# Optimization experiments

Measured on AMD Instinct MI355X. Metric: run time of the kernel, lower is better.

The kernel has to match this reference:

```python
import jax, jax.numpy as jnp
import numpy as np

B, T, V, H, C = 128, 4096, 128, 256, 10
EPS = 0.1  # args._epsilon (training mode)

def setup_inputs() -> dict:
    key = jax.random.key(0)
    ks = jax.random.split(key, 8)
    rn = lambda k, shape, sc: (jax.random.normal(k, shape, jnp.float32) * sc)
    return {
        "X": rn(ks[0], (B, T, V), 1.0),
        "u": jax.random.uniform(ks[1], (B, T, 1), jnp.float32),
        "Wk": rn(ks[2], (V, 4 * H), 0.05),
        "Wr": rn(ks[3], (H, 4 * H), 0.05),
        "b_lstm": jnp.zeros((4 * H,), jnp.float32),
        "Wo": rn(ks[4], (H, C), 0.05),
        "bo": jnp.zeros((C,), jnp.float32),
        "Wc": rn(ks[5], (H + 1, 1), 0.05),
        "bc": jnp.zeros((1,), jnp.float32),
        "Wb": rn(ks[6], (H + 1, 1), 0.05),
        "bb": jnp.zeros((1,), jnp.float32),
    }

def reference(X, u, Wk, Wr, b_lstm, Wo, bo, Wc, bc, Wb, bb):
    Bn = X.shape[0]
    xT = jnp.swapaxes(X, 0, 1)  # [T,B,V]
    uT = jnp.swapaxes(u, 0, 1)  # [T,B,1]
    ts = jnp.arange(T, dtype=jnp.float32)

    def step(carry, inp):
        h, c, preds, halt = carry
        x_t, u_t, t = inp
        # Keras LSTMCell: gates order i, f, g(c), o
        z = x_t @ Wk + h @ Wr + b_lstm  # [B,4H]
        i, f, g, o = jnp.split(z, 4, axis=1)
        i = jax.nn.sigmoid(i); f = jax.nn.sigmoid(f)
        g = jnp.tanh(g); o = jax.nn.sigmoid(o)
        c = f * c + i * g
        h = o * jnp.tanh(c)
        logits = jax.nn.softmax(h @ Wo + bo, axis=-1)  # softmax Dense
        time = jnp.ones((Bn, 1), jnp.float32) * t
        c_in = jax.lax.stop_gradient(jnp.concatenate([h, time], axis=1))
        p = jax.nn.sigmoid(c_in @ Wc + bc)
        probs = (1.0 - EPS) * p + EPS * 0.05
        a = (u_t < probs).astype(jnp.float32)  # Bernoulli sample via uniform noise
        _b = c_in @ Wb + bb  # baseline (does not affect returned logits)
        preds = jnp.where((a == 1.0) & (preds == 0.0), logits, preds)
        halt = jnp.where((halt == -1.0) & (a == 1.0), time, halt)
        return (h, c, preds, halt), logits

    init = (jnp.zeros((Bn, H), jnp.float32),
            jnp.zeros((Bn, H), jnp.float32),
            jnp.zeros((Bn, C), jnp.float32),
            -jnp.ones((Bn, 1), jnp.float32))
    (h, c, preds, halt), all_logits = jax.lax.scan(step, init, (xT, uT, ts))
    logits_last = all_logits[-1]
    # samples that never halted get the final-step logits
    return jnp.where(preds == 0.0, logits_last, preds)
```

## Files before the change

### kernel.cpp

```cpp
#include <hip/hip_runtime.h>
#include <cstddef>
#include <cstdint>

#define NT_ 4096
#define NV_ 128
#define NH_ 256
#define NC_ 10
#define KT_ 384
#define NGRP 16
#define SB   8
#define GWG  16
#define TPW  256
#define VST  12
#define Z9   9
#define FULLMASK 255

#define SM_W    0
#define SM_V    24576
#define SM_ZP   (SM_V + KT_*VST)
#define SM_C    (SM_ZP + 2304)
#define SM_BL   (SM_C + 144)
#define SM_WC   (SM_BL + 64)
#define SM_WO   (SM_WC + 260)
#define SM_HD   (SM_WO + 2560)
#define SM_RED  (SM_HD + 12)
#define SM_TOT  (SM_RED + 32)
#define SMEM_BYTES (SM_TOT * 4)

#define WS_HBUF  4096
#define WS_DIAG  (1u << 20)

#define ALD(p)    __hip_atomic_load((p), __ATOMIC_RELAXED, __HIP_MEMORY_SCOPE_AGENT)
#define AST(p,v)  __hip_atomic_store((p), (v), __ATOMIC_RELAXED, __HIP_MEMORY_SCOPE_AGENT)

#define FMA8(S) \
  acc[S].x = fmaf(w4.x, vs, acc[S].x); \
  acc[S].y = fmaf(w4.y, vs, acc[S].y); \
  acc[S].z = fmaf(w4.z, vs, acc[S].z); \
  acc[S].w = fmaf(w4.w, vs, acc[S].w);

#define ZSTEP(i)                                            \
  {                                                         \
    float4 w4 = wl4[(i) * 256 + wbase];                     \
    const float* vk = v_lds + ((i) * 16 + ks) * VST;        \
    float4 va = *(const float4*)(vk);                       \
    float4 vb = *(const float4*)(vk + 4);                   \
    { float vs = va.x; FMA8(0) } { float vs = va.y; FMA8(1) } \
    { float vs = va.z; FMA8(2) } { float vs = va.w; FMA8(3) } \
    { float vs = vb.x; FMA8(4) } { float vs = vb.y; FMA8(5) } \
    { float vs = vb.z; FMA8(6) } { float vs = vb.w; FMA8(7) } \
  }

extern "C" __global__ __launch_bounds__(TPW, 1)
void earliest_coop(const float* __restrict__ X, const float* __restrict__ U,
                   const float* __restrict__ Wk, const float* __restrict__ Wr,
                   const float* __restrict__ bl, const float* __restrict__ Wo,
                   const float* __restrict__ bo, const float* __restrict__ Wc,
                   const float* __restrict__ bc, float* __restrict__ out,
                   int* __restrict__ cnt, float* __restrict__ hbuf,
                   char* __restrict__ diag)
{
  extern __shared__ float smem[];
  float* w_lds = smem + SM_W;
  float* v_lds = smem + SM_V;
  float* zp    = smem + SM_ZP;
  float* c_lds = smem + SM_C;
  float* bl_s  = smem + SM_BL;
  float* wc_s  = smem + SM_WC;
  float* wo_s  = smem + SM_WO;
  float* hd_s  = smem + SM_HD;
  float* red   = smem + SM_RED;
  __shared__ int halted_lds;
  __shared__ int wflags;

  const int tid  = threadIdx.x;
  const int w    = blockIdx.x & 15;
  const int g    = blockIdx.x >> 4;
  const int colq = tid & 15;
  const int ks   = tid >> 4;
  const bool leader = (w == 0);

  for (int m = 0; m < 24; ++m) {
    int idx4 = m * 256 + tid;
    int k = idx4 >> 4, cq = idx4 & 15;
    int rr = cq >> 2, qq = cq & 3;
    int col4 = rr * 64 + w * 4 + qq;
    float4 wv;
    if (k < NV_) wv = ((const float4*)Wk)[(size_t)k * 256 + col4];
    else         wv = ((const float4*)Wr)[(size_t)(k - NV_) * 256 + col4];
    ((float4*)w_lds)[k * 16 + (cq ^ (k & 7))] = wv;
  }
  if (tid < 64) {
    int rr = tid >> 4, e = tid & 15;
    bl_s[tid] = bl[rr * 256 + w * 16 + e];
  }
  wc_s[tid] = Wc[tid];
  if (tid == 0) wc_s[256] = Wc[256];
  if (tid < 128) c_lds[(tid >> 3) * Z9 + (tid & 7)] = 0.f;
  if (leader) {
    for (int m = tid; m < NH_ * NC_; m += TPW) wo_s[m] = Wo[m];
  }
  if (tid < 10)  hd_s[tid] = bo[tid];
  if (tid == 10) hd_s[10] = bc[0];
  if (tid == 0)  { halted_lds = 0; wflags = 0; }

  int* cntg = cnt + (g << 6);
  const int cswz  = colq ^ (ks & 7);
  const int wbase = ks * 16 + cswz;
  const float4* wl4 = (const float4*)w_lds;

  const int xk4 = tid >> 3;
  const int xs  = tid & 7;
  const float4* X4 = (const float4*)X;
  float4 xr = X4[((size_t)(g * SB + xs) * NT_ + 0) * 32 + xk4];

  __syncthreads();
  {
    #pragma unroll
    for (int j = 0; j < 4; ++j)
      v_lds[(4 * xk4 + j) * VST + xs] = ((const float*)&xr)[j];
  }
  __syncthreads();

  float4 acc[8];
  #pragma unroll
  for (int s = 0; s < 8; ++s) acc[s] = make_float4(0.f, 0.f, 0.f, 0.f);
  #pragma unroll
  for (int i = 0; i < 8; ++i) ZSTEP(i)

  float uv_pf = 0.f;

  for (int it = 0;; ++it) {
    if (tid == 0) wflags = 0;
    if (it == 0) {
      #pragma unroll
      for (int i2 = 0; i2 < 8; ++i2) {
        int flat = i2 * 256 + tid;
        v_lds[(NV_ + (flat >> 3)) * VST + (flat & 7)] = 0.f;
      }
    } else {
      const float* hsrc = hbuf + ((size_t)(it & 1) * NGRP + g) * NH_ * SB;
      #pragma unroll
      for (int i2 = 0; i2 < 8; ++i2) {
        int flat = i2 * 256 + tid;
        v_lds[(NV_ + (flat >> 3)) * VST + (flat & 7)] = ALD(hsrc + flat);
      }
    }
    __syncthreads();

    if (it < NT_) {
      if (it + 1 < NT_)
        xr = X4[((size_t)(g * SB + xs) * NT_ + (it + 1)) * 32 + xk4];
      #pragma unroll
      for (int i = 8; i < 24; ++i) ZSTEP(i)
      #pragma unroll
      for (int off = 16; off <= 32; off <<= 1) {
        #pragma unroll
        for (int s = 0; s < 8; ++s) {
          acc[s].x += __shfl_xor(acc[s].x, off, 64);
          acc[s].y += __shfl_xor(acc[s].y, off, 64);
          acc[s].z += __shfl_xor(acc[s].z, off, 64);
          acc[s].w += __shfl_xor(acc[s].w, off, 64);
        }
      }
      if ((tid & 48) == 0) {
        int w4 = tid >> 6;
        float4* zp4 = (float4*)zp;
        #pragma unroll
        for (int s = 0; s < 8; ++s) zp4[(w4 * 16 + colq) * Z9 + s] = acc[s];
      }
    }
    if (it >= 1) {
      const float* hv = v_lds + (NV_ + tid) * VST;
      const float wcv = wc_s[tid];
      float part[SB];
      #pragma unroll
      for (int s = 0; s < SB; ++s) part[s] = hv[s] * wcv;
      #pragma unroll
      for (int off = 1; off <= 32; off <<= 1) {
        #pragma unroll
        for (int s = 0; s < SB; ++s) part[s] += __shfl_xor(part[s], off, 64);
      }
      if ((tid & 63) == 0) {
        int w4 = tid >> 6;
        #pragma unroll
        for (int s = 0; s < SB; ++s) red[w4 * 8 + s] = part[s];
      }
      if (tid >= 128 && tid < 128 + SB)
        uv_pf = U[(size_t)(g * SB + (tid - 128)) * NT_ + (it - 1)];
    }
    __syncthreads();

    if (it < NT_ && tid < 128) {
      int e = tid >> 3, s = tid & 7;
      float zg4[4];
      #pragma unroll
      for (int r = 0; r < 4; ++r) {
        int cq = r * 4 + (e >> 2);
        int j  = e & 3;
        float sum = 0.f;
        #pragma unroll
        for (int w4 = 0; w4 < 4; ++w4)
          sum += zp[((w4 * 16 + cq) * Z9 + s) * 4 + j];
        zg4[r] = sum + bl_s[r * 16 + e];
      }
      float gi = 1.f / (1.f + expf(-zg4[0]));
      float gf = 1.f / (1.f + expf(-zg4[1]));
      float gg = tanhf(zg4[2]);
      float go = 1.f / (1.f + expf(-zg4[3]));
      float c = gf * c_lds[e * Z9 + s] + gi * gg;
      c_lds[e * Z9 + s] = c;
      float h = go * tanhf(c);
      size_t hidx = (((size_t)((it + 1) & 1) * NGRP + g) * NH_ + (w * 16 + e)) * SB + s;
      AST(hbuf + hidx, h);
    }
    if (it >= 1 && tid >= 128 && tid < 128 + SB) {
      const int s_ = tid - 128;
      if (!((halted_lds >> s_) & 1)) {
        const int tau = it - 1;
        const float psum = red[0 * 8 + s_] + red[1 * 8 + s_] + red[2 * 8 + s_] + red[3 * 8 + s_];
        const float pre   = psum + (float)tau * wc_s[256] + hd_s[10];
        const float p     = 1.f / (1.f + expf(-pre));
        const float probs = 0.9f * p + 0.005f;
        const bool  a     = (uv_pf < probs);
        if (a || tau == NT_ - 1) atomicOr(&wflags, 1 << s_);
        if (a) atomicOr(&halted_lds, 1 << s_);
      }
    }
    __syncthreads();

    if (tid == 0) {
      __hip_atomic_fetch_add(cntg, 1, __ATOMIC_RELAXED, __HIP_MEMORY_SCOPE_AGENT);
      if (diag)
        __builtin_nontemporal_store(1u,
            (uint32_t*)(diag + (((size_t)blockIdx.x << 8) + (it & 255)) * 64));
    }

    if (it + 1 < NT_) {
      #pragma unroll
      for (int j = 0; j < 4; ++j)
        v_lds[(4 * xk4 + j) * VST + xs] = ((const float*)&xr)[j];
    }

    if (it >= 1 && leader && wflags) {
      const int e5 = tid >> 3, s = tid & 7;
      float accv[NC_];
      #pragma unroll
      for (int cc = 0; cc < NC_; ++cc) accv[cc] = 0.f;
      #pragma unroll
      for (int i2 = 0; i2 < 8; ++i2) {
        const int e = i2 * 32 + e5;
        const float hvv = v_lds[(NV_ + e) * VST + s];
        #pragma unroll
        for (int cc = 0; cc < NC_; ++cc) accv[cc] += hvv * wo_s[e * NC_ + cc];
      }
      #pragma unroll
      for (int off = 8; off <= 32; off <<= 1) {
        #pragma unroll
        for (int cc = 0; cc < NC_; ++cc) accv[cc] += __shfl_xor(accv[cc], off, 64);
      }
      if ((tid & 56) == 0) {
        const int w4 = tid >> 6;
        #pragma unroll
        for (int cc = 0; cc < NC_; ++cc) zp[(w4 * 8 + s) * NC_ + cc] = accv[cc];
      }
      __syncthreads();
      if (tid < SB && ((wflags >> tid) & 1)) {
        const int s_ = tid;
        float l[NC_];
        float mx = -1e30f;
        #pragma unroll
        for (int cc = 0; cc < NC_; ++cc) {
          l[cc] = zp[(0 * 8 + s_) * NC_ + cc] + zp[(1 * 8 + s_) * NC_ + cc]
                + zp[(2 * 8 + s_) * NC_ + cc] + zp[(3 * 8 + s_) * NC_ + cc] + hd_s[cc];
          mx = fmaxf(mx, l[cc]);
        }
        float ssum = 0.f;
        #pragma unroll
        for (int cc = 0; cc < NC_; ++cc) { l[cc] = expf(l[cc] - mx); ssum += l[cc]; }
        const float inv = 1.f / ssum;
        float* op = out + (g * SB + s_) * NC_;
        #pragma unroll
        for (int cc = 0; cc < NC_; ++cc) op[cc] = l[cc] * inv;
      }
      __syncthreads();
    }

    if (halted_lds == FULLMASK || it == NT_) break;

    __syncthreads();

    #pragma unroll
    for (int s = 0; s < 8; ++s) acc[s] = make_float4(0.f, 0.f, 0.f, 0.f);
    if (it + 1 < NT_) {
      #pragma unroll
      for (int i = 0; i < 8; ++i) ZSTEP(i)
    }

    if (tid == 0) {
      const int target = GWG * (it + 1);
      while (ALD(cntg) < target) __builtin_amdgcn_s_sleep(1);
    }
    __syncthreads();
  }
}

extern "C" void kernel_launch(void* const* d_in, const int* in_sizes, int n_in,
                              void* d_out, int out_size, void* d_ws, size_t ws_size,
                              hipStream_t stream)
{
  const float* X  = (const float*)d_in[0];
  const float* U  = (const float*)d_in[1];
  const float* Wk = (const float*)d_in[2];
  const float* Wr = (const float*)d_in[3];
  const float* bL = (const float*)d_in[4];
  const float* Wo = (const float*)d_in[5];
  const float* bo = (const float*)d_in[6];
  const float* Wc = (const float*)d_in[7];
  const float* bc = (const float*)d_in[8];
  float* out = (float*)d_out;

  int*   cnt  = (int*)d_ws;
  float* hbuf = (float*)((char*)d_ws + WS_HBUF);
  char*  diag = (ws_size >= (6u << 20)) ? ((char*)d_ws + WS_DIAG) : nullptr;

  hipMemsetAsync(d_ws, 0, WS_HBUF, stream);

  hipFuncSetAttribute((const void*)earliest_coop,
                      hipFuncAttributeMaxDynamicSharedMemorySize, SMEM_BYTES);

  void* args[] = { (void*)&X, (void*)&U, (void*)&Wk, (void*)&Wr, (void*)&bL,
                   (void*)&Wo, (void*)&bo, (void*)&Wc, (void*)&bc, (void*)&out,
                   (void*)&cnt, (void*)&hbuf, (void*)&diag };
  hipError_t lerr = hipLaunchCooperativeKernel((const void*)earliest_coop,
                                               dim3(NGRP * GWG), dim3(TPW),
                                               args, SMEM_BYTES, stream);
  if (lerr != hipSuccess) {
    hipLaunchKernelGGL(earliest_coop, dim3(NGRP * GWG), dim3(TPW), SMEM_BYTES, stream,
                       X, U, Wk, Wr, bL, Wo, bo, Wc, bc, out, cnt, hbuf, diag);
  }
}
```

Baseline: 181.4 us.

## Replace group counter barrier with step-tagged hidden-state flags

The per-group atomic counter and spin barrier are replaced by 64-bit slots that pack each hidden value with its step index. Each thread polls only the eight values it needs until their tags match the current step, then writes them straight into LDS. This fuses data exchange and synchronisation into one round trip and removes the separate counter increment, its polling, and the reload pass at the top of each step. In exchange it moves twice the bytes per hidden value, every thread now spins on global memory instead of one, and correctness depends on the tag and data being written atomically in a single 64-bit store.

```diff
diff --git a/kernel.cpp b/kernel.cpp
--- a/kernel.cpp
+++ b/kernel.cpp
@@ -27,11 +27,11 @@
 #define SM_TOT  (SM_RED + 32)
 #define SMEM_BYTES (SM_TOT * 4)
 
-#define WS_HBUF  4096
-#define WS_DIAG  (1u << 20)
-
-#define ALD(p)    __hip_atomic_load((p), __ATOMIC_RELAXED, __HIP_MEMORY_SCOPE_AGENT)
-#define AST(p,v)  __hip_atomic_store((p), (v), __ATOMIC_RELAXED, __HIP_MEMORY_SCOPE_AGENT)
+#define WS_HQ_BYTES (512u * 1024u)
+#define WS_DIAG     (1u << 20)
+
+#define AQLD(p)   __hip_atomic_load((p),  __ATOMIC_RELAXED, __HIP_MEMORY_SCOPE_AGENT)
+#define AQST(p,v) __hip_atomic_store((p), (v), __ATOMIC_RELAXED, __HIP_MEMORY_SCOPE_AGENT)
 
 #define FMA8(S) \
   acc[S].x = fmaf(w4.x, vs, acc[S].x); \
@@ -57,8 +57,7 @@
                    const float* __restrict__ bl, const float* __restrict__ Wo,
                    const float* __restrict__ bo, const float* __restrict__ Wc,
                    const float* __restrict__ bc, float* __restrict__ out,
-                   int* __restrict__ cnt, float* __restrict__ hbuf,
-                   char* __restrict__ diag)
+                   unsigned long long* __restrict__ hq, char* __restrict__ diag)
 {
   extern __shared__ float smem[];
   float* w_lds = smem + SM_W;
@@ -104,10 +103,14 @@
   if (tid == 10) hd_s[10] = bc[0];
   if (tid == 0)  { halted_lds = 0; wflags = 0; }
 
-  int* cntg = cnt + (g << 6);
-  const int cswz  = colq ^ (ks & 7);
-  const int wbase = ks * 16 + cswz;
+  const int wbase = ks * 16 + (colq ^ (ks & 7));
   const float4* wl4 = (const float4*)w_lds;
+
+  unsigned long long* hq_me =
+      hq + (size_t)g * 2048 + (size_t)(w * 16 + (tid >> 3)) * 8 + (tid & 7);
+  unsigned long long* hq_my =
+      hq + (size_t)g * 2048 + (size_t)tid * 8;
+  const size_t HQP = (size_t)NGRP * 2048;
 
   const int xk4 = tid >> 3;
   const int xs  = tid & 7;
@@ -119,6 +122,11 @@
     #pragma unroll
     for (int j = 0; j < 4; ++j)
       v_lds[(4 * xk4 + j) * VST + xs] = ((const float*)&xr)[j];
+    #pragma unroll
+    for (int i2 = 0; i2 < 8; ++i2) {
+      int flat = i2 * 256 + tid;
+      v_lds[(NV_ + (flat >> 3)) * VST + (flat & 7)] = 0.f;
+    }
   }
   __syncthreads();
 
@@ -131,22 +139,7 @@
   float uv_pf = 0.f;
 
   for (int it = 0;; ++it) {
-    if (tid == 0) wflags = 0;
-    if (it == 0) {
-      #pragma unroll
-      for (int i2 = 0; i2 < 8; ++i2) {
-        int flat = i2 * 256 + tid;
-        v_lds[(NV_ + (flat >> 3)) * VST + (flat & 7)] = 0.f;
-      }
-    } else {
-      const float* hsrc = hbuf + ((size_t)(it & 1) * NGRP + g) * NH_ * SB;
-      #pragma unroll
-      for (int i2 = 0; i2 < 8; ++i2) {
-        int flat = i2 * 256 + tid;
-        v_lds[(NV_ + (flat >> 3)) * VST + (flat & 7)] = ALD(hsrc + flat);
-      }
-    }
-    __syncthreads();
+    if (tid == 192) wflags = 0;
 
     if (it < NT_) {
       if (it + 1 < NT_)
@@ -211,8 +204,10 @@
       float c = gf * c_lds[e * Z9 + s] + gi * gg;
       c_lds[e * Z9 + s] = c;
       float h = go * tanhf(c);
-      size_t hidx = (((size_t)((it + 1) & 1) * NGRP + g) * NH_ + (w * 16 + e)) * SB + s;
-      AST(hbuf + hidx, h);
+      unsigned long long unit =
+          (unsigned long long)__float_as_uint(h) |
+          ((unsigned long long)(unsigned)(it + 1) << 32);
+      AQST(hq_me + (size_t)((it + 1) & 1) * HQP, unit);
     }
     if (it >= 1 && tid >= 128 && tid < 128 + SB) {
       const int s_ = tid - 128;
@@ -229,19 +224,16 @@
     }
     __syncthreads();
 
-    if (tid == 0) {
-      __hip_atomic_fetch_add(cntg, 1, __ATOMIC_RELAXED, __HIP_MEMORY_SCOPE_AGENT);
-      if (diag)
-        __builtin_nontemporal_store(1u,
-            (uint32_t*)(diag + (((size_t)blockIdx.x << 8) + (it & 255)) * 64));
-    }
-
+    if (tid == 0 && diag && it >= 8 && it < 128) {
+      char* dl = diag + (((size_t)blockIdx.x) << 14) + (size_t)(it - 8) * 128;
+      __builtin_nontemporal_store(1u, (uint32_t*)dl);
+      __builtin_nontemporal_store(1u, (uint32_t*)(dl + 64));
+    }
     if (it + 1 < NT_) {
       #pragma unroll
       for (int j = 0; j < 4; ++j)
         v_lds[(4 * xk4 + j) * VST + xs] = ((const float*)&xr)[j];
     }
-
     if (it >= 1 && leader && wflags) {
       const int e5 = tid >> 3, s = tid & 7;
       float accv[NC_];
@@ -297,9 +289,26 @@
       for (int i = 0; i < 8; ++i) ZSTEP(i)
     }
 
-    if (tid == 0) {
-      const int target = GWG * (it + 1);
-      while (ALD(cntg) < target) __builtin_amdgcn_s_sleep(1);
+    {
+      const unsigned long long* src = hq_my + (size_t)((it + 1) & 1) * HQP;
+      const unsigned want = (unsigned)(it + 1);
+      unsigned long long uq[8];
+      unsigned pend = 0xffu;
+      for (;;) {
+        #pragma unroll
+        for (int j = 0; j < 8; ++j) {
+          if ((pend >> j) & 1) {
+            uq[j] = AQLD(src + j);
+            if ((unsigned)(uq[j] >> 32) == want) pend &= ~(1u << j);
+          }
+        }
+        if (!pend) break;
+        __builtin_amdgcn_s_sleep(1);
+      }
+      float* dst = v_lds + (NV_ + tid) * VST;
+      #pragma unroll
+      for (int j = 0; j < 8; ++j)
+        dst[j] = __uint_as_float((unsigned)uq[j]);
     }
     __syncthreads();
   }
@@ -320,23 +329,22 @@
   const float* bc = (const float*)d_in[8];
   float* out = (float*)d_out;
 
-  int*   cnt  = (int*)d_ws;
-  float* hbuf = (float*)((char*)d_ws + WS_HBUF);
-  char*  diag = (ws_size >= (6u << 20)) ? ((char*)d_ws + WS_DIAG) : nullptr;
-
-  hipMemsetAsync(d_ws, 0, WS_HBUF, stream);
+  unsigned long long* hq = (unsigned long long*)d_ws;
+  char* diag = (ws_size >= (6u << 20)) ? ((char*)d_ws + WS_DIAG) : nullptr;
+
+  hipMemsetAsync(d_ws, 0, WS_HQ_BYTES, stream);
 
   hipFuncSetAttribute((const void*)earliest_coop,
                       hipFuncAttributeMaxDynamicSharedMemorySize, SMEM_BYTES);
 
   void* args[] = { (void*)&X, (void*)&U, (void*)&Wk, (void*)&Wr, (void*)&bL,
                    (void*)&Wo, (void*)&bo, (void*)&Wc, (void*)&bc, (void*)&out,
-                   (void*)&cnt, (void*)&hbuf, (void*)&diag };
+                   (void*)&hq, (void*)&diag };
   hipError_t lerr = hipLaunchCooperativeKernel((const void*)earliest_coop,
                                                dim3(NGRP * GWG), dim3(TPW),
                                                args, SMEM_BYTES, stream);
   if (lerr != hipSuccess) {
     hipLaunchKernelGGL(earliest_coop, dim3(NGRP * GWG), dim3(TPW), SMEM_BYTES, stream,
-                       X, U, Wk, Wr, bL, Wo, bo, Wc, bc, out, cnt, hbuf, diag);
+                       X, U, Wk, Wr, bL, Wo, bo, Wc, bc, out, hq, diag);
   }
 }
```

After: 180.3 us. Within noise of the previous version (-0.6%).
